# Kernel optimization log

Measured on AMD Instinct MI355X. Metric: run time of the kernel, lower is better.

## Reference

```python
import jax, jax.numpy as jnp
from jax import lax
import numpy as np

S, ST, CI, K = 3, 2, 64, 7  # num_subset_S, num_subset_T, inter_channels, kernel_size


def _ln2(x, g, b, eps=1e-5):
    # LayerNorm over the last TWO dims (matches normalized_shape=[L, C])
    m = x.mean(axis=(-2, -1), keepdims=True)
    v = x.var(axis=(-2, -1), keepdims=True)
    return (x - m) / jnp.sqrt(v + eps) * g + b


def setup_inputs() -> dict:
    key = jax.random.key(0)
    ks = jax.random.split(key, 8)
    N, V, T, C = 32, 25, 64, 256
    g = lambda i, shape: jax.random.normal(ks[i], shape, jnp.float32) * 0.02
    return {
        "x": jax.random.normal(ks[0], (N, V, T, C), jnp.float32),
        "Wqk_s": g(1, (C, 2 * S * CI)), "bqk_s": jnp.zeros((2 * S * CI,), jnp.float32),
        "alphas": jnp.ones((1, 1, 1, S), jnp.float32),
        "attention0s": jnp.ones((1, V, V, S), jnp.float32) / V,
        "Wo_s": g(2, (S * C, C)), "bo_s": jnp.zeros((C,), jnp.float32),
        "g_os": jnp.ones((T, C), jnp.float32), "b_os": jnp.zeros((T, C), jnp.float32),
        "Wff_s": g(3, (C, C)), "bff_s": jnp.zeros((C,), jnp.float32),
        "g_ffs": jnp.ones((T, C), jnp.float32), "b_ffs": jnp.zeros((T, C), jnp.float32),
        "Wqk_t": g(4, (C, 4 * ST * CI)), "bqk_t": jnp.zeros((4 * ST * CI,), jnp.float32),
        "alphat_f": jnp.ones((1, 1, 1, ST), jnp.float32),
        "alphat_b": jnp.ones((1, 1, 1, ST), jnp.float32),
        "Wo_t": g(5, (2 * ST * C, C)), "bo_t": jnp.zeros((C,), jnp.float32),
        "g_ot": jnp.ones((V, C), jnp.float32), "b_ot": jnp.zeros((V, C), jnp.float32),
        "Wff_t": g(6, (C, C)), "bff_t": jnp.zeros((C,), jnp.float32),
        "g_fft": jnp.ones((V, C), jnp.float32), "b_fft": jnp.zeros((V, C), jnp.float32),
        "conv_w": g(7, (C, C, K, 1)), "conv_b": jnp.zeros((C,), jnp.float32),
        "bn_g": jnp.ones((C,), jnp.float32), "bn_b": jnp.zeros((C,), jnp.float32),
        "bn_m": jnp.zeros((C,), jnp.float32), "bn_v": jnp.ones((C,), jnp.float32),
    }


def reference(x, Wqk_s, bqk_s, alphas, attention0s, Wo_s, bo_s, g_os, b_os,
              Wff_s, bff_s, g_ffs, b_ffs, Wqk_t, bqk_t, alphat_f, alphat_b,
              Wo_t, bo_t, g_ot, b_ot, Wff_t, bff_t, g_fft, b_fft,
              conv_w, conv_b, bn_g, bn_b, bn_m, bn_v):
    N, V, T, C = x.shape
    gelu = lambda a: jax.nn.gelu(a, approximate=False)
    # ---- spatial multi-subset attention ----
    qk = (x @ Wqk_s + bqk_s).reshape(N, V, T, CI, 2 * S)
    q, k = qk[..., :S], qk[..., S:]
    att = jnp.tanh(jnp.einsum('nutcs,nvtcs->nuvs', q, k) / (CI * T)) * alphas + attention0s
    y = jnp.einsum('nutc,nuvs->nvtcs', x, att).reshape(N, V, T, S * C)
    y = gelu(x + _ln2(y @ Wo_s + bo_s, g_os, b_os))       # out_nets + residual (downs1=id)
    y = gelu(x + _ln2(y @ Wff_s + bff_s, g_ffs, b_ffs))   # ff_nets  + residual (downs2=id)
    y = y.transpose(0, 2, 1, 3)                            # (N,T,V,C)
    # ---- directed temporal attention ----
    qkt = (y @ Wqk_t + bqk_t).reshape(N, T, V, CI, 4 * ST)
    q_f, q_b = qkt[..., :ST], qkt[..., ST:2 * ST]
    k_f, k_b = qkt[..., 2 * ST:3 * ST], qkt[..., 3 * ST:]
    bmask = jnp.triu(jnp.ones((T, T), x.dtype))            # backward_mask; forward = transpose
    att_b = jnp.tanh(jnp.einsum('ntvcs,nqvcs->ntqs', q_b, k_b) / (CI * V)) * alphat_b * bmask[None, :, :, None]
    att_f = jnp.tanh(jnp.einsum('ntvcs,nqvcs->ntqs', q_f, k_f) / (CI * V)) * alphat_f * bmask.T[None, :, :, None]
    z_f = jnp.einsum('ntvc,ntqs->nqvcs', y, att_f).reshape(N, T, V, ST * C)
    z_b = jnp.einsum('ntvc,ntqs->nqvcs', y, att_b).reshape(N, T, V, ST * C)
    z = jnp.concatenate([z_f, z_b], axis=-1)               # (N,T,V,4C)
    z = gelu(y + _ln2(z @ Wo_t + bo_t, g_ot, b_ot))        # out_nett + residual (downt1=id)
    z = gelu(y + _ln2(z @ Wff_t + bff_t, g_fft, b_fft))    # ff_nett  + residual (downt2=id)
    # ---- TCN tail: (N,T,V,C) -> nctv ----
    zc = z.transpose(0, 3, 1, 2)                           # (N,C,T,V)
    pad = (K - 1) // 2
    z1 = lax.conv_general_dilated(zc, conv_w, (1, 1), [(pad, pad), (0, 0)],
                                  dimension_numbers=('NCHW', 'OIHW', 'NCHW'))
    z1 = z1 + conv_b[None, :, None, None]
    z1 = (z1 - bn_m[None, :, None, None]) / jnp.sqrt(bn_v + 1e-5)[None, :, None, None]
    z1 = z1 * bn_g[None, :, None, None] + bn_b[None, :, None, None]  # BatchNorm2d (eval)
    z1 = gelu(zc + z1)                                     # downt3 = identity
    return z1.transpose(0, 3, 2, 1)                        # nctv -> nvtc, (N,V,T,C)
```

## Files before the change

### kernel.cpp

```cpp
#include <hip/hip_runtime.h>

static constexpr int N_ = 32, V_ = 25, T_ = 64, C_ = 256;
static constexpr int S_ = 3, ST_ = 2, CI_ = 64, K_ = 7;
static constexpr int M_  = N_ * V_ * T_;
static constexpr int TC_ = T_ * C_;
static constexpr int VC_ = V_ * C_;
static constexpr long TOT_ = (long)M_ * C_;
static constexpr long PLANE_ = 2048L * 1600;
static constexpr int TP_ = T_ + 6;

typedef __bf16 bf16x8 __attribute__((ext_vector_type(8)));
typedef float  f32x4  __attribute__((ext_vector_type(4)));

__device__ __forceinline__ float gelu_f(float x) {
    return 0.5f * x * (1.0f + erff(x * 0.70710678118654752f));
}
__device__ __forceinline__ ushort f2bf(float x) {
    uint u = __float_as_uint(x);
    u += 0x7fffu + ((u >> 16) & 1u);
    return (ushort)(u >> 16);
}
__device__ __forceinline__ float bf2f(ushort h) { return __uint_as_float((uint)h << 16); }

__device__ __forceinline__ int lofs(int row, int chunk) {
    return row * 32 + ((chunk ^ ((row >> 1) & 3)) << 3);
}

__device__ __forceinline__ void gll16(const ushort* g, ushort* l) {
    __builtin_amdgcn_global_load_lds(
        (const __attribute__((address_space(1))) void*)g,
        (__attribute__((address_space(3))) void*)l, 16, 0, 0);
}

__device__ __forceinline__ void xcd_swz(int& bx, int& by) {
    const int gx = gridDim.x;
    const int nwg = gx * gridDim.y;
    const int o = blockIdx.y * gx + blockIdx.x;
    const int q = nwg >> 3, r = nwg & 7;
    const int xcd = o & 7, idx = o >> 3;
    const int id = (xcd < r) ? (xcd * (q + 1) + idx)
                             : (r * (q + 1) + (xcd - r) * q + idx);
    bx = id % gx; by = id / gx;
}

__global__ void prep_w(const float* __restrict__ W, int Kc, int Nc,
                       ushort* __restrict__ hi, ushort* __restrict__ lo) {
    int idx = blockIdx.x * 256 + threadIdx.x;
    if (idx >= Kc * Nc) return;
    int n = idx / Kc, k = idx % Kc;
    float x = W[(long)k * Nc + n];
    ushort h = f2bf(x);
    hi[idx] = h;
    lo[idx] = f2bf(x - bf2f(h));
}
__global__ void prep_conv(const float* __restrict__ cw,
                          ushort* __restrict__ hi, ushort* __restrict__ lo) {
    int idx = blockIdx.x * 256 + threadIdx.x;
    if (idx >= K_ * C_ * C_) return;
    int kh = idx / (C_ * C_);
    int rem = idx % (C_ * C_);
    int o = rem >> 8, i = rem & 255;
    float x = cw[((long)o * C_ + i) * K_ + kh];
    ushort h = f2bf(x);
    hi[idx] = h;
    lo[idx] = f2bf(x - bf2f(h));
}
__global__ void prep_x(const float* __restrict__ X,
                       ushort* __restrict__ Xh, ushort* __restrict__ Xl) {
    long i = (long)blockIdx.x * 256 + threadIdx.x;
    if (i >= TOT_) return;
    float v = X[i];
    ushort h = f2bf(v);
    Xh[i] = h;
    Xl[i] = f2bf(v - bf2f(h));
}
__global__ void zero_pad(ushort* __restrict__ Zph, ushort* __restrict__ Zpl) {
    int idx = blockIdx.x * 256 + threadIdx.x;
    if (idx >= N_ * 6 * V_ * C_) return;
    int n = idx / (6 * V_ * C_);
    int rem = idx % (6 * V_ * C_);
    int tpi = rem / (V_ * C_), vc = rem % (V_ * C_);
    int tp = (tpi < 3) ? tpi : (64 + tpi);
    long o = ((long)(n * TP_ + tp) * V_) * C_ + vc;
    Zph[o] = 0; Zpl[o] = 0;
}

__global__ __launch_bounds__(256) void gemm_bf(
    const ushort* __restrict__ Agh, const ushort* __restrict__ Agl,
    const ushort* __restrict__ Wh,  const ushort* __restrict__ Wl,
    const float* __restrict__ bias,
    float* __restrict__ Out, int Nc)
{
    __shared__ ushort Ah[128 * 32], Al[128 * 32], Bh[128 * 32], Bl[128 * 32];
    int bx, by;  xcd_swz(bx, by);
    const int tid = threadIdx.x;
    const int row0 = by * 128, col0 = bx * 128;
    const int lane = tid & 63;
    const int wid = tid >> 6, wm = wid >> 1, wn = wid & 1;
    const int fr = lane & 15, fc = lane >> 4;
    const int r0 = tid >> 2;
    const int cl0 = (tid & 3) ^ ((r0 >> 1) & 3);
    const int r1 = r0 + 64;
    const int cl1 = (tid & 3) ^ ((r1 >> 1) & 3);
    const long a0off = (long)(row0 + r0) * 256 + cl0 * 8;
    const long a1off = (long)(row0 + r1) * 256 + cl1 * 8;
    const long w0off = (long)(col0 + r0) * 256 + cl0 * 8;
    const long w1off = (long)(col0 + r1) * 256 + cl1 * 8;
    ushort* dA0 = &Ah[tid * 8];         ushort* dA1 = &Ah[(tid + 256) * 8];
    ushort* dL0 = &Al[tid * 8];         ushort* dL1 = &Al[(tid + 256) * 8];
    ushort* dB0 = &Bh[tid * 8];         ushort* dB1 = &Bh[(tid + 256) * 8];
    ushort* dM0 = &Bl[tid * 8];         ushort* dM1 = &Bl[(tid + 256) * 8];

    f32x4 acc[4][4] = {};
    for (int k0 = 0; k0 < 256; k0 += 32) {
        __syncthreads();
        gll16(Agh + a0off + k0, dA0);  gll16(Agh + a1off + k0, dA1);
        gll16(Agl + a0off + k0, dL0);  gll16(Agl + a1off + k0, dL1);
        gll16(Wh  + w0off + k0, dB0);  gll16(Wh  + w1off + k0, dB1);
        gll16(Wl  + w0off + k0, dM0);  gll16(Wl  + w1off + k0, dM1);
        __syncthreads();
        bf16x8 fah[4], fal[4];
        #pragma unroll
        for (int i = 0; i < 4; ++i) {
            int oA = lofs(wm * 64 + i * 16 + fr, fc);
            fah[i] = *(bf16x8*)&Ah[oA];
            fal[i] = *(bf16x8*)&Al[oA];
        }
        #pragma unroll
        for (int j = 0; j < 4; ++j) {
            int oW = lofs(wn * 64 + j * 16 + fr, fc);
            bf16x8 wh = *(bf16x8*)&Bh[oW];
            bf16x8 wl = *(bf16x8*)&Bl[oW];
            #pragma unroll
            for (int i = 0; i < 4; ++i) {
                acc[i][j] = __builtin_amdgcn_mfma_f32_16x16x32_bf16(fah[i], wh, acc[i][j], 0, 0, 0);
                acc[i][j] = __builtin_amdgcn_mfma_f32_16x16x32_bf16(fah[i], wl, acc[i][j], 0, 0, 0);
                acc[i][j] = __builtin_amdgcn_mfma_f32_16x16x32_bf16(fal[i], wh, acc[i][j], 0, 0, 0);
            }
        }
    }
    float bv[4]; int colv[4];
    #pragma unroll
    for (int j = 0; j < 4; ++j) {
        colv[j] = col0 + wn * 64 + j * 16 + fr;
        bv[j] = bias ? bias[colv[j]] : 0.0f;
    }
    #pragma unroll
    for (int i = 0; i < 4; ++i) {
        long rbase = row0 + wm * 64 + i * 16 + fc * 4;
        #pragma unroll
        for (int r = 0; r < 4; ++r) {
            long ob = (rbase + r) * (long)Nc;
            #pragma unroll
            for (int j = 0; j < 4; ++j)
                Out[ob + colv[j]] = acc[i][j][r] + bv[j];
        }
    }
}

__global__ __launch_bounds__(256) void conv_bn_gelu(
    const ushort* __restrict__ Zph, const ushort* __restrict__ Zpl,
    const ushort* __restrict__ Wh, const ushort* __restrict__ Wl,
    const float* __restrict__ conv_b, const float* __restrict__ bn_g,
    const float* __restrict__ bn_b,  const float* __restrict__ bn_m,
    const float* __restrict__ bn_v,
    float* __restrict__ Out)
{
    __shared__ ushort Ah[128 * 32], Al[128 * 32], Bh[128 * 32], Bl[128 * 32];
    int bx, by;  xcd_swz(bx, by);
    const int tid = threadIdx.x;
    const int row0 = by * 128, col0 = bx * 128;
    const int lane = tid & 63;
    const int wid = tid >> 6, wm = wid >> 1, wn = wid & 1;
    const int fr = lane & 15, fc = lane >> 4;
    const int r0 = tid >> 2;
    const int cl0 = (tid & 3) ^ ((r0 >> 1) & 3);
    const int r1 = r0 + 64;
    const int cl1 = (tid & 3) ^ ((r1 >> 1) & 3);
    const int m0 = row0 + r0, m1 = row0 + r1;
    const int n0 = m0 / (T_ * V_), q0 = m0 % (T_ * V_);
    const int n1 = m1 / (T_ * V_), q1 = m1 % (T_ * V_);
    const long a0base = ((long)(n0 * TP_ + q0 / V_) * V_ + q0 % V_) * 256 + cl0 * 8;
    const long a1base = ((long)(n1 * TP_ + q1 / V_) * V_ + q1 % V_) * 256 + cl1 * 8;
    const long w0base = (long)(col0 + r0) * 256 + cl0 * 8;
    const long w1base = (long)(col0 + r1) * 256 + cl1 * 8;
    ushort* dA0 = &Ah[tid * 8];         ushort* dA1 = &Ah[(tid + 256) * 8];
    ushort* dL0 = &Al[tid * 8];         ushort* dL1 = &Al[(tid + 256) * 8];
    ushort* dB0 = &Bh[tid * 8];         ushort* dB1 = &Bh[(tid + 256) * 8];
    ushort* dM0 = &Bl[tid * 8];         ushort* dM1 = &Bl[(tid + 256) * 8];

    f32x4 acc[4][4] = {};
    for (int kt = 0; kt < K_ * 8; ++kt) {
        const int kh = kt >> 3;
        const long kc = (kt & 7) * 32;
        const long ao = (long)kh * V_ * 256;
        const long wo = (long)kh * 65536 + kc;
        __syncthreads();
        gll16(Zph + a0base + ao + kc, dA0);  gll16(Zph + a1base + ao + kc, dA1);
        gll16(Zpl + a0base + ao + kc, dL0);  gll16(Zpl + a1base + ao + kc, dL1);
        gll16(Wh + w0base + wo, dB0);        gll16(Wh + w1base + wo, dB1);
        gll16(Wl + w0base + wo, dM0);        gll16(Wl + w1base + wo, dM1);
        __syncthreads();
        bf16x8 fah[4], fal[4];
        #pragma unroll
        for (int i = 0; i < 4; ++i) {
            int oA = lofs(wm * 64 + i * 16 + fr, fc);
            fah[i] = *(bf16x8*)&Ah[oA];
            fal[i] = *(bf16x8*)&Al[oA];
        }
        #pragma unroll
        for (int j = 0; j < 4; ++j) {
            int oW = lofs(wn * 64 + j * 16 + fr, fc);
            bf16x8 wh = *(bf16x8*)&Bh[oW];
            bf16x8 wl = *(bf16x8*)&Bl[oW];
            #pragma unroll
            for (int i = 0; i < 4; ++i) {
                acc[i][j] = __builtin_amdgcn_mfma_f32_16x16x32_bf16(fah[i], wh, acc[i][j], 0, 0, 0);
                acc[i][j] = __builtin_amdgcn_mfma_f32_16x16x32_bf16(fah[i], wl, acc[i][j], 0, 0, 0);
                acc[i][j] = __builtin_amdgcn_mfma_f32_16x16x32_bf16(fal[i], wh, acc[i][j], 0, 0, 0);
            }
        }
    }
    float cbv[4], scv[4], shv[4]; int colv[4];
    #pragma unroll
    for (int j = 0; j < 4; ++j) {
        int c = col0 + wn * 64 + j * 16 + fr;
        colv[j] = c;
        cbv[j] = conv_b[c];
        float sc = rsqrtf(bn_v[c] + 1e-5f) * bn_g[c];
        scv[j] = sc;
        shv[j] = bn_b[c] - bn_m[c] * sc;
    }
    #pragma unroll
    for (int i = 0; i < 4; ++i)
        #pragma unroll
        for (int r = 0; r < 4; ++r) {
            int m = row0 + wm * 64 + i * 16 + fc * 4 + r;
            int n = m / (T_ * V_);
            int rem = m % (T_ * V_);
            int t = rem / V_, v = rem % V_;
            long ob = (((long)n * V_ + v) * T_ + t) * C_;
            long pb = ((long)(n * TP_ + t + 3) * V_ + v) * C_;
            #pragma unroll
            for (int j = 0; j < 4; ++j) {
                float cv = acc[i][j][r] + cbv[j];
                float bn = cv * scv[j] + shv[j];
                float res = bf2f(Zph[pb + colv[j]]) + bf2f(Zpl[pb + colv[j]]);
                Out[ob + colv[j]] = gelu_f(res + bn);
            }
        }
}

__global__ void zero_f32(float* __restrict__ p, int n) {
    int i = blockIdx.x * 256 + threadIdx.x;
    if (i < n) p[i] = 0.0f;
}

__global__ __launch_bounds__(256) void att_s_partial(
    const float* __restrict__ QK,
    float* __restrict__ attPre)
{
    const int n = blockIdx.x;
    const int tg = blockIdx.y;
    __shared__ float lds[V_ * 385];
    const int NOUT = V_ * V_ * S_;
    float acc[8] = {};
    for (int ttc = 0; ttc < 4; ++ttc) {
        int t = tg * 4 + ttc;
        __syncthreads();
        for (int l = threadIdx.x; l < V_ * 96; l += 256) {
            int v = l / 96, j = (l % 96) * 4;
            float4 q = *(const float4*)&QK[(((long)n * V_ + v) * T_ + t) * 384 + j];
            float* d = &lds[v * 385 + j];
            d[0] = q.x; d[1] = q.y; d[2] = q.z; d[3] = q.w;
        }
        __syncthreads();
        int ai = 0;
        for (int o = threadIdx.x; o < NOUT; o += 256, ++ai) {
            int u = o / (V_ * S_), rem = o % (V_ * S_), v = rem / S_, s = rem % S_;
            const float* qp = &lds[u * 385 + s];
            const float* kp = &lds[v * 385 + S_ + s];
            float sum = 0.f;
            #pragma unroll 8
            for (int ci = 0; ci < CI_; ++ci) sum += qp[ci * 6] * kp[ci * 6];
            acc[ai] += sum;
        }
    }
    int ai = 0;
    for (int o = threadIdx.x; o < NOUT; o += 256, ++ai)
        atomicAdd(&attPre[(long)n * NOUT + o], acc[ai]);
}

__global__ void att_s_final(const float* __restrict__ attPre,
                            const float* __restrict__ alphas,
                            const float* __restrict__ att0,
                            float* __restrict__ attS) {
    int idx = blockIdx.x * 256 + threadIdx.x;
    if (idx >= N_ * V_ * V_ * S_) return;
    int o = idx % (V_ * V_ * S_);
    int s = o % S_;
    attS[idx] = tanhf(attPre[idx] * (1.0f / (CI_ * T_))) * alphas[s] + att0[o];
}

__global__ __launch_bounds__(256) void vmix_all(
    const float* __restrict__ G,
    const float* __restrict__ attS,
    const float* __restrict__ bias,
    float* __restrict__ P)
{
    const int n = blockIdx.y;
    const int t = blockIdx.x;
    const int c = threadIdx.x;
    __shared__ float a[3][V_ * V_];
    for (int l = threadIdx.x; l < V_ * V_ * S_; l += 256) {
        int uv = l / S_, s = l % S_;
        a[s][uv] = attS[((long)n * V_ * V_ + uv) * S_ + s];
    }
    __syncthreads();
    float acc[V_] = {};
    for (int u = 0; u < V_; ++u) {
        const float* g = G + ((long)((n * V_ + u) * T_) + t) * 768 + c;
        float v0 = g[0], v1 = g[256], v2 = g[512];
        const float* a0 = &a[0][u * V_], *a1 = &a[1][u * V_], *a2 = &a[2][u * V_];
        #pragma unroll
        for (int v = 0; v < V_; ++v)
            acc[v] += a0[v] * v0 + a1[v] * v1 + a2[v] * v2;
    }
    const float b = bias[c];
    for (int v = 0; v < V_; ++v)
        P[((long)(n * V_ + v) * T_ + t) * C_ + c] = acc[v] + b;
}

__global__ void qkt_repack(const float* __restrict__ QKT,
                           ushort* __restrict__ QPh, ushort* __restrict__ QPl) {
    long idx = (long)blockIdx.x * 256 + threadIdx.x;
    if (idx >= (long)M_ * CI_) return;
    int m = (int)(idx >> 6), ci = (int)(idx & 63);
    int n = m / (T_ * V_);
    int rem = m % (T_ * V_);
    int t = rem / V_, v = rem % V_;
    const float* src = QKT + (long)m * 512 + ci * 8;
    float4 s0 = *(const float4*)src;
    float4 s1 = *(const float4*)(src + 4);
    float f[8] = {s0.x, s0.y, s0.z, s0.w, s1.x, s1.y, s1.z, s1.w};
    long rowk = ((long)(n * T_ + t)) * 1600 + v * 64 + ci;
    #pragma unroll
    for (int chan = 0; chan < 8; ++chan) {
        ushort h = f2bf(f[chan]);
        QPh[(long)chan * PLANE_ + rowk] = h;
        QPl[(long)chan * PLANE_ + rowk] = f2bf(f[chan] - bf2f(h));
    }
}

__global__ __launch_bounds__(256) void att_t_mfma(
    const ushort* __restrict__ QPh, const ushort* __restrict__ QPl,
    float* __restrict__ part)
{
    const int ks = blockIdx.x, pair = blockIdx.y, n = blockIdx.z;
    const int kbeg = (ks * 50) / 4, kend = ((ks + 1) * 50) / 4;
    __shared__ ushort Qh[64 * 32], Ql[64 * 32], Kh[64 * 32], Kl[64 * 32];
    const int tid = threadIdx.x;
    const int lane = tid & 63;
    const int wid = tid >> 6, wm = wid >> 1, wn = wid & 1;
    const int fr = lane & 15, fc = lane >> 4;
    const int tr = tid >> 2, tc = tid & 3;
    const long rowoff = ((long)n * T_ + tr) * 1600 + tc * 8;
    const ushort* qh_g = QPh + (long)pair * PLANE_ + rowoff;
    const ushort* ql_g = QPl + (long)pair * PLANE_ + rowoff;
    const ushort* kh_g = QPh + (long)(pair + 4) * PLANE_ + rowoff;
    const ushort* kl_g = QPl + (long)(pair + 4) * PLANE_ + rowoff;
    const int la = lofs(tr, tc);

    uint4 pqh = *(const uint4*)(qh_g + kbeg * 32);
    uint4 pql = *(const uint4*)(ql_g + kbeg * 32);
    uint4 pkh = *(const uint4*)(kh_g + kbeg * 32);
    uint4 pkl = *(const uint4*)(kl_g + kbeg * 32);

    f32x4 acc[2][2] = {};
    for (int kstep = kbeg; kstep < kend; ++kstep) {
        __syncthreads();
        *(uint4*)&Qh[la] = pqh;  *(uint4*)&Ql[la] = pql;
        *(uint4*)&Kh[la] = pkh;  *(uint4*)&Kl[la] = pkl;
        __syncthreads();
        if (kstep + 1 < kend) {
            pqh = *(const uint4*)(qh_g + (kstep + 1) * 32);
            pql = *(const uint4*)(ql_g + (kstep + 1) * 32);
            pkh = *(const uint4*)(kh_g + (kstep + 1) * 32);
            pkl = *(const uint4*)(kl_g + (kstep + 1) * 32);
        }
        bf16x8 ah[2], al[2];
        #pragma unroll
        for (int i = 0; i < 2; ++i) {
            int oA = lofs(wm * 32 + i * 16 + fr, fc);
            ah[i] = *(bf16x8*)&Qh[oA];
            al[i] = *(bf16x8*)&Ql[oA];
        }
        #pragma unroll
        for (int j = 0; j < 2; ++j) {
            int oB = lofs(wn * 32 + j * 16 + fr, fc);
            bf16x8 bh = *(bf16x8*)&Kh[oB];
            bf16x8 bl = *(bf16x8*)&Kl[oB];
            #pragma unroll
            for (int i = 0; i < 2; ++i) {
                acc[i][j] = __builtin_amdgcn_mfma_f32_16x16x32_bf16(ah[i], bh, acc[i][j], 0, 0, 0);
                acc[i][j] = __builtin_amdgcn_mfma_f32_16x16x32_bf16(ah[i], bl, acc[i][j], 0, 0, 0);
                acc[i][j] = __builtin_amdgcn_mfma_f32_16x16x32_bf16(al[i], bh, acc[i][j], 0, 0, 0);
            }
        }
    }
    float* pb = part + (((long)ks * N_ + n) * 4 + pair) * 4096;
    #pragma unroll
    for (int i = 0; i < 2; ++i)
        #pragma unroll
        for (int r = 0; r < 4; ++r) {
            int t = wm * 32 + i * 16 + fc * 4 + r;
            #pragma unroll
            for (int j = 0; j < 2; ++j) {
                int q = wn * 32 + j * 16 + fr;
                pb[t * 64 + q] = acc[i][j][r];
            }
        }
}

__global__ void att_t_final(const float* __restrict__ part,
                            const float* __restrict__ alphat_f,
                            const float* __restrict__ alphat_b,
                            float* __restrict__ attF, float* __restrict__ attB) {
    int idx = blockIdx.x * 256 + threadIdx.x;
    if (idx >= N_ * 4 * 4096) return;
    int n = idx >> 14;
    int rem = idx & 16383;
    int p = rem >> 12, tq = rem & 4095;
    int t = tq >> 6, q = tq & 63;
    const long stride = (long)N_ * 4 * 4096;
    float sum = 0.f;
    #pragma unroll
    for (int ks = 0; ks < 4; ++ks) sum += part[ks * stride + idx];
    float val = tanhf(sum * (1.0f / (CI_ * V_)));
    if (p < 2) {
        float m = (t >= q) ? 1.0f : 0.0f;
        attF[((long)(n * 2 + p)) * 4096 + tq] = val * alphat_f[p] * m;
    } else {
        float m = (q >= t) ? 1.0f : 0.0f;
        attB[((long)(n * 2 + (p - 2))) * 4096 + tq] = val * alphat_b[p - 2] * m;
    }
}

template <bool INIT>
__global__ __launch_bounds__(256) void tmix_all(
    const float* __restrict__ G,
    const float* __restrict__ att,
    const float* __restrict__ bias,
    float* __restrict__ P)
{
    const int n = blockIdx.y;
    const int col = blockIdx.x * 64 + (threadIdx.x & 63);
    const int ty = threadIdx.x >> 6;
    const int v = col >> 8, c = col & 255;
    __shared__ float a[2 * T_ * T_];
    for (int l = threadIdx.x; l < 2 * T_ * T_; l += 256)
        a[l] = att[(long)n * 2 * T_ * T_ + l];
    __syncthreads();
    float acc[16] = {};
    for (int t = 0; t < T_; ++t) {
        const float* g = G + ((long)((n * T_ + t) * V_) + v) * 512 + c;
        float v0 = g[0], v1 = g[256];
        const float* ar0 = &a[t * T_ + ty * 16];
        const float* ar1 = ar0 + T_ * T_;
        #pragma unroll
        for (int i = 0; i < 16; ++i) acc[i] += ar0[i] * v0 + ar1[i] * v1;
    }
    for (int i = 0; i < 16; ++i) {
        int q = ty * 16 + i;
        long idx = ((long)n * T_ + q) * VC_ + col;
        if (INIT) P[idx] = acc[i] + bias[c];
        else      P[idx] += acc[i];
    }
}

#define LN_STATS(PBASE, L)                                                     \
    float s = 0.f, ss = 0.f;                                                   \
    for (int i = threadIdx.x; i < L; i += 256) { float a = (PBASE)[i]; s += a; ss += a * a; } \
    __shared__ float rs[4], rss[4];                                            \
    _Pragma("unroll")                                                          \
    for (int off = 32; off > 0; off >>= 1) { s += __shfl_down(s, off); ss += __shfl_down(ss, off); } \
    if ((threadIdx.x & 63) == 0) { rs[threadIdx.x >> 6] = s; rss[threadIdx.x >> 6] = ss; } \
    __syncthreads();                                                           \
    s = rs[0] + rs[1] + rs[2] + rs[3];                                         \
    ss = rss[0] + rss[1] + rss[2] + rss[3];                                    \
    const float mean = s * (1.0f / (L));                                       \
    const float var  = ss * (1.0f / (L)) - mean * mean;                        \
    const float rstd = rsqrtf(var + 1e-5f);

__global__ __launch_bounds__(256) void ln_tc_y(
    const float* __restrict__ P, const float* __restrict__ X,
    const float* __restrict__ G, const float* __restrict__ B,
    ushort* __restrict__ Oh, ushort* __restrict__ Ol)
{
    const int g = blockIdx.x;
    const float* p = P + (long)g * TC_;
    const float* x = X + (long)g * TC_;
    LN_STATS(p, TC_)
    for (int i = threadIdx.x; i < TC_; i += 256) {
        float val = (p[i] - mean) * rstd * G[i] + B[i];
        float r = gelu_f(x[i] + val);
        ushort h = f2bf(r);
        Oh[(long)g * TC_ + i] = h;
        Ol[(long)g * TC_ + i] = f2bf(r - bf2f(h));
    }
}

__global__ __launch_bounds__(256) void ln_tc_yt(
    const float* __restrict__ P, const float* __restrict__ X,
    const float* __restrict__ G, const float* __restrict__ B,
    ushort* __restrict__ Oh, ushort* __restrict__ Ol)
{
    const int g = blockIdx.x;
    const int n = g / V_, v = g % V_;
    const float* p = P + (long)g * TC_;
    const float* x = X + (long)g * TC_;
    LN_STATS(p, TC_)
    for (int i = threadIdx.x; i < TC_; i += 256) {
        float val = (p[i] - mean) * rstd * G[i] + B[i];
        float r = gelu_f(x[i] + val);
        int t = i >> 8, c = i & 255;
        long o = (((long)n * T_ + t) * V_ + v) * C_ + c;
        ushort h = f2bf(r);
        Oh[o] = h;
        Ol[o] = f2bf(r - bf2f(h));
    }
}

__global__ __launch_bounds__(256) void ln_vc_z(
    const float* __restrict__ P,
    const ushort* __restrict__ Xh, const ushort* __restrict__ Xl,
    const float* __restrict__ G, const float* __restrict__ B,
    ushort* __restrict__ Oh, ushort* __restrict__ Ol)
{
    const int g = blockIdx.x;
    const float* p = P + (long)g * VC_;
    LN_STATS(p, VC_)
    for (int i = threadIdx.x; i < VC_; i += 256) {
        long o = (long)g * VC_ + i;
        float xr = bf2f(Xh[o]) + bf2f(Xl[o]);
        float val = (p[i] - mean) * rstd * G[i] + B[i];
        float r = gelu_f(xr + val);
        ushort h = f2bf(r);
        Oh[o] = h;
        Ol[o] = f2bf(r - bf2f(h));
    }
}

__global__ __launch_bounds__(256) void ln_vc_z2(
    const float* __restrict__ P,
    const ushort* __restrict__ Xh, const ushort* __restrict__ Xl,
    const float* __restrict__ G, const float* __restrict__ B,
    ushort* __restrict__ Zph, ushort* __restrict__ Zpl)
{
    const int g = blockIdx.x;
    const int n = g / T_, t = g % T_;
    const float* p = P + (long)g * VC_;
    LN_STATS(p, VC_)
    const long pbase = ((long)(n * TP_ + t + 3) * V_) * C_;
    for (int i = threadIdx.x; i < VC_; i += 256) {
        long o = (long)g * VC_ + i;
        float xr = bf2f(Xh[o]) + bf2f(Xl[o]);
        float val = (p[i] - mean) * rstd * G[i] + B[i];
        float r = gelu_f(xr + val);
        ushort h = f2bf(r);
        Zph[pbase + i] = h;
        Zpl[pbase + i] = f2bf(r - bf2f(h));
    }
}

extern "C" void kernel_launch(void* const* d_in, const int* in_sizes, int n_in,
                              void* d_out, int out_size, void* d_ws, size_t ws_size,
                              hipStream_t stream)
{
    const float* x        = (const float*)d_in[0];
    const float* Wqk_s    = (const float*)d_in[1];
    const float* bqk_s    = (const float*)d_in[2];
    const float* alphas   = (const float*)d_in[3];
    const float* att0s    = (const float*)d_in[4];
    const float* Wo_s     = (const float*)d_in[5];
    const float* bo_s     = (const float*)d_in[6];
    const float* g_os     = (const float*)d_in[7];
    const float* b_os     = (const float*)d_in[8];
    const float* Wff_s    = (const float*)d_in[9];
    const float* bff_s    = (const float*)d_in[10];
    const float* g_ffs    = (const float*)d_in[11];
    const float* b_ffs    = (const float*)d_in[12];
    const float* Wqk_t    = (const float*)d_in[13];
    const float* bqk_t    = (const float*)d_in[14];
    const float* alphat_f = (const float*)d_in[15];
    const float* alphat_b = (const float*)d_in[16];
    const float* Wo_t     = (const float*)d_in[17];
    const float* bo_t     = (const float*)d_in[18];
    const float* g_ot     = (const float*)d_in[19];
    const float* b_ot     = (const float*)d_in[20];
    const float* Wff_t    = (const float*)d_in[21];
    const float* bff_t    = (const float*)d_in[22];
    const float* g_fft    = (const float*)d_in[23];
    const float* b_fft    = (const float*)d_in[24];
    const float* conv_w   = (const float*)d_in[25];
    const float* conv_b   = (const float*)d_in[26];
    const float* bn_g     = (const float*)d_in[27];
    const float* bn_b     = (const float*)d_in[28];
    const float* bn_m     = (const float*)d_in[29];
    const float* bn_v     = (const float*)d_in[30];

    float* Bp  = (float*)d_ws;
    float* R0f = Bp;
    float* R1f = Bp + TOT_;
    float* R2f = Bp + 2 * TOT_;
    float* R3f = Bp + 3 * TOT_;
    float* SM  = Bp + 4 * TOT_;
    float* attPre = SM;
    float* attS   = attPre + N_*V_*V_*S_;
    float* attF   = attS   + N_*V_*V_*S_;
    float* attB   = attF   + (long)N_*2*T_*T_;
    float* part   = attB   + (long)N_*2*T_*T_;
    ushort* wp = (ushort*)(part + 4L*N_*4*4096);
    ushort* qs_h = wp;  wp += 384*256;   ushort* qs_l = wp;  wp += 384*256;
    ushort* os_h = wp;  wp += 768*256;   ushort* os_l = wp;  wp += 768*256;
    ushort* fs_h = wp;  wp += 256*256;   ushort* fs_l = wp;  wp += 256*256;
    ushort* qt_h = wp;  wp += 512*256;   ushort* qt_l = wp;  wp += 512*256;
    ushort* ot0_h= wp;  wp += 512*256;   ushort* ot0_l= wp;  wp += 512*256;
    ushort* ot1_h= wp;  wp += 512*256;   ushort* ot1_l= wp;  wp += 512*256;
    ushort* ft_h = wp;  wp += 256*256;   ushort* ft_l = wp;  wp += 256*256;
    ushort* cv_h = wp;  wp += K_*256*256; ushort* cv_l = wp;

    ushort* xh  = (ushort*)R3f;  ushort* xl  = xh  + TOT_;
    ushort* Yh  = (ushort*)R0f;  ushort* Yl  = Yh  + TOT_;
    ushort* YTh = (ushort*)d_out; ushort* YTl = YTh + TOT_;
    ushort* QPh = (ushort*)R2f;  ushort* QPl = (ushort*)R3f;
    ushort* Zh  = (ushort*)R0f;  ushort* Zl  = Zh  + TOT_;
    ushort* Zph = (ushort*)R1f;
    ushort* Zpl = Zph + (long)N_ * TP_ * V_ * C_;

    auto prepw = [&](const float* W, int Nc, ushort* h, ushort* l) {
        prep_w<<<(256*Nc + 255)/256, 256, 0, stream>>>(W, 256, Nc, h, l);
    };
    prepw(Wqk_s, 384, qs_h, qs_l);
    prepw(Wo_s,  768, os_h, os_l);
    prepw(Wff_s, 256, fs_h, fs_l);
    prepw(Wqk_t, 512, qt_h, qt_l);
    prepw(Wo_t,                   512, ot0_h, ot0_l);
    prepw(Wo_t + (long)ST_*C_*C_, 512, ot1_h, ot1_l);
    prepw(Wff_t, 256, ft_h, ft_l);
    prep_conv<<<(K_*C_*C_ + 255)/256, 256, 0, stream>>>(conv_w, cv_h, cv_l);
    prep_x<<<(int)((TOT_ + 255)/256), 256, 0, stream>>>(x, xh, xl);

    gemm_bf<<<dim3(3, 400), 256, 0, stream>>>(xh, xl, qs_h, qs_l, bqk_s, R0f, 384);
    zero_f32<<<(N_*V_*V_*S_ + 255)/256, 256, 0, stream>>>(attPre, N_*V_*V_*S_);
    att_s_partial<<<dim3(N_, 16), 256, 0, stream>>>(R0f, attPre);
    att_s_final<<<(N_*V_*V_*S_ + 255)/256, 256, 0, stream>>>(attPre, alphas, att0s, attS);
    gemm_bf<<<dim3(6, 400), 256, 0, stream>>>(xh, xl, os_h, os_l, nullptr, R0f, 768);
    vmix_all<<<dim3(T_, N_), 256, 0, stream>>>(R0f, attS, bo_s, R3f);
    ln_tc_y<<<N_*V_, 256, 0, stream>>>(R3f, x, g_os, b_os, Yh, Yl);
    gemm_bf<<<dim3(2, 400), 256, 0, stream>>>(Yh, Yl, fs_h, fs_l, bff_s, R1f, 256);
    ln_tc_yt<<<N_*V_, 256, 0, stream>>>(R1f, x, g_ffs, b_ffs, YTh, YTl);

    gemm_bf<<<dim3(4, 400), 256, 0, stream>>>(YTh, YTl, qt_h, qt_l, bqk_t, R0f, 512);
    qkt_repack<<<(int)(((long)M_*CI_ + 255)/256), 256, 0, stream>>>(R0f, QPh, QPl);
    att_t_mfma<<<dim3(4, 4, N_), 256, 0, stream>>>(QPh, QPl, part);
    att_t_final<<<(N_*4*4096 + 255)/256, 256, 0, stream>>>(part, alphat_f, alphat_b, attF, attB);
    gemm_bf<<<dim3(4, 400), 256, 0, stream>>>(YTh, YTl, ot0_h, ot0_l, nullptr, R0f, 512);
    tmix_all<true><<<dim3(VC_/64, N_), 256, 0, stream>>>(R0f, attF, bo_t, R2f);
    gemm_bf<<<dim3(4, 400), 256, 0, stream>>>(YTh, YTl, ot1_h, ot1_l, nullptr, R0f, 512);
    tmix_all<false><<<dim3(VC_/64, N_), 256, 0, stream>>>(R0f, attB, nullptr, R2f);
    ln_vc_z<<<N_*T_, 256, 0, stream>>>(R2f, YTh, YTl, g_ot, b_ot, Zh, Zl);
    gemm_bf<<<dim3(2, 400), 256, 0, stream>>>(Zh, Zl, ft_h, ft_l, bff_t, R3f, 256);
    zero_pad<<<(N_*6*V_*C_ + 255)/256, 256, 0, stream>>>(Zph, Zpl);
    ln_vc_z2<<<N_*T_, 256, 0, stream>>>(R3f, YTh, YTl, g_fft, b_fft, Zph, Zpl);

    conv_bn_gelu<<<dim3(2, 400), 256, 0, stream>>>(Zph, Zpl, cv_h, cv_l, conv_b, bn_g, bn_b, bn_m, bn_v, (float*)d_out);
}
```

Measured before the change: 1.266 ms.

## Double-buffer LDS in GEMM and conv kernels, merge weight-prep launches

The bf16 split-precision GEMM and the conv GEMM now use two LDS buffers per operand, so the global-to-LDS load of the next K slice is issued before the MFMAs on the current slice. This drops one of the two barriers per iteration and aims to hide load latency behind compute. The eight weight-preparation launches are merged into one kernel that dispatches on a flat index, which removes launch overhead. LDS use doubles to 64 KB per block, which may lower occupancy.

```diff
diff --git a/kernel.cpp b/kernel.cpp
--- a/kernel.cpp
+++ b/kernel.cpp
@@ -43,27 +43,45 @@
     bx = id % gx; by = id / gx;
 }
 
-__global__ void prep_w(const float* __restrict__ W, int Kc, int Nc,
-                       ushort* __restrict__ hi, ushort* __restrict__ lo) {
+__global__ void prep_weights(
+    const float* __restrict__ Wqk_s, const float* __restrict__ Wo_s,
+    const float* __restrict__ Wff_s, const float* __restrict__ Wqk_t,
+    const float* __restrict__ Wo_t,  const float* __restrict__ Wff_t,
+    const float* __restrict__ conv_w,
+    ushort* __restrict__ qs_h, ushort* __restrict__ qs_l,
+    ushort* __restrict__ os_h, ushort* __restrict__ os_l,
+    ushort* __restrict__ fs_h, ushort* __restrict__ fs_l,
+    ushort* __restrict__ qt_h, ushort* __restrict__ qt_l,
+    ushort* __restrict__ ot0_h, ushort* __restrict__ ot0_l,
+    ushort* __restrict__ ot1_h, ushort* __restrict__ ot1_l,
+    ushort* __restrict__ ft_h, ushort* __restrict__ ft_l,
+    ushort* __restrict__ cv_h, ushort* __restrict__ cv_l)
+{
     int idx = blockIdx.x * 256 + threadIdx.x;
-    if (idx >= Kc * Nc) return;
-    int n = idx / Kc, k = idx % Kc;
-    float x = W[(long)k * Nc + n];
-    ushort h = f2bf(x);
-    hi[idx] = h;
-    lo[idx] = f2bf(x - bf2f(h));
-}
-__global__ void prep_conv(const float* __restrict__ cw,
-                          ushort* __restrict__ hi, ushort* __restrict__ lo) {
-    int idx = blockIdx.x * 256 + threadIdx.x;
-    if (idx >= K_ * C_ * C_) return;
-    int kh = idx / (C_ * C_);
-    int rem = idx % (C_ * C_);
-    int o = rem >> 8, i = rem & 255;
-    float x = cw[((long)o * C_ + i) * K_ + kh];
-    ushort h = f2bf(x);
-    hi[idx] = h;
-    lo[idx] = f2bf(x - bf2f(h));
+    float x; ushort *h, *l; int li;
+    if (idx < 819200) {
+        const float* W; int base, ldw;
+        if      (idx <  98304) { W=Wqk_s; h=qs_h;  l=qs_l;  base=0;      ldw=384; }
+        else if (idx < 294912) { W=Wo_s;  h=os_h;  l=os_l;  base=98304;  ldw=768; }
+        else if (idx < 360448) { W=Wff_s; h=fs_h;  l=fs_l;  base=294912; ldw=256; }
+        else if (idx < 491520) { W=Wqk_t; h=qt_h;  l=qt_l;  base=360448; ldw=512; }
+        else if (idx < 622592) { W=Wo_t;  h=ot0_h; l=ot0_l; base=491520; ldw=512; }
+        else if (idx < 753664) { W=Wo_t + (long)ST_*C_*C_; h=ot1_h; l=ot1_l; base=622592; ldw=512; }
+        else                   { W=Wff_t; h=ft_h;  l=ft_l;  base=753664; ldw=256; }
+        li = idx - base;
+        int n = li >> 8, k = li & 255;
+        x = W[(long)k * ldw + n];
+    } else {
+        li = idx - 819200;
+        int kh = li / (C_ * C_);
+        int rem = li % (C_ * C_);
+        int o = rem >> 8, i = rem & 255;
+        x = conv_w[((long)o * C_ + i) * K_ + kh];
+        h = cv_h; l = cv_l;
+    }
+    ushort hb = f2bf(x);
+    h[li] = hb;
+    l[li] = f2bf(x - bf2f(hb));
 }
 __global__ void prep_x(const float* __restrict__ X,
                        ushort* __restrict__ Xh, ushort* __restrict__ Xl) {
@@ -91,7 +109,8 @@
     const float* __restrict__ bias,
     float* __restrict__ Out, int Nc)
 {
-    __shared__ ushort Ah[128 * 32], Al[128 * 32], Bh[128 * 32], Bl[128 * 32];
+    __shared__ ushort Ah[2][128 * 32], Al[2][128 * 32];
+    __shared__ ushort Bh[2][128 * 32], Bl[2][128 * 32];
     int bx, by;  xcd_swz(bx, by);
     const int tid = threadIdx.x;
     const int row0 = by * 128, col0 = bx * 128;
@@ -106,31 +125,33 @@
     const long a1off = (long)(row0 + r1) * 256 + cl1 * 8;
     const long w0off = (long)(col0 + r0) * 256 + cl0 * 8;
     const long w1off = (long)(col0 + r1) * 256 + cl1 * 8;
-    ushort* dA0 = &Ah[tid * 8];         ushort* dA1 = &Ah[(tid + 256) * 8];
-    ushort* dL0 = &Al[tid * 8];         ushort* dL1 = &Al[(tid + 256) * 8];
-    ushort* dB0 = &Bh[tid * 8];         ushort* dB1 = &Bh[(tid + 256) * 8];
-    ushort* dM0 = &Bl[tid * 8];         ushort* dM1 = &Bl[(tid + 256) * 8];
+    const int u0 = tid * 8, u1 = (tid + 256) * 8;
+
+    auto stage = [&](int b, int k0) {
+        gll16(Agh + a0off + k0, &Ah[b][u0]);  gll16(Agh + a1off + k0, &Ah[b][u1]);
+        gll16(Agl + a0off + k0, &Al[b][u0]);  gll16(Agl + a1off + k0, &Al[b][u1]);
+        gll16(Wh  + w0off + k0, &Bh[b][u0]);  gll16(Wh  + w1off + k0, &Bh[b][u1]);
+        gll16(Wl  + w0off + k0, &Bl[b][u0]);  gll16(Wl  + w1off + k0, &Bl[b][u1]);
+    };
 
     f32x4 acc[4][4] = {};
-    for (int k0 = 0; k0 < 256; k0 += 32) {
-        __syncthreads();
-        gll16(Agh + a0off + k0, dA0);  gll16(Agh + a1off + k0, dA1);
-        gll16(Agl + a0off + k0, dL0);  gll16(Agl + a1off + k0, dL1);
-        gll16(Wh  + w0off + k0, dB0);  gll16(Wh  + w1off + k0, dB1);
-        gll16(Wl  + w0off + k0, dM0);  gll16(Wl  + w1off + k0, dM1);
-        __syncthreads();
+    stage(0, 0);
+    __syncthreads();
+    int cur = 0;
+    for (int ks = 0; ks < 8; ++ks) {
+        if (ks + 1 < 8) stage(cur ^ 1, (ks + 1) * 32);
         bf16x8 fah[4], fal[4];
         #pragma unroll
         for (int i = 0; i < 4; ++i) {
             int oA = lofs(wm * 64 + i * 16 + fr, fc);
-            fah[i] = *(bf16x8*)&Ah[oA];
-            fal[i] = *(bf16x8*)&Al[oA];
+            fah[i] = *(bf16x8*)&Ah[cur][oA];
+            fal[i] = *(bf16x8*)&Al[cur][oA];
         }
         #pragma unroll
         for (int j = 0; j < 4; ++j) {
             int oW = lofs(wn * 64 + j * 16 + fr, fc);
-            bf16x8 wh = *(bf16x8*)&Bh[oW];
-            bf16x8 wl = *(bf16x8*)&Bl[oW];
+            bf16x8 wh = *(bf16x8*)&Bh[cur][oW];
+            bf16x8 wl = *(bf16x8*)&Bl[cur][oW];
             #pragma unroll
             for (int i = 0; i < 4; ++i) {
                 acc[i][j] = __builtin_amdgcn_mfma_f32_16x16x32_bf16(fah[i], wh, acc[i][j], 0, 0, 0);
@@ -138,6 +159,8 @@
                 acc[i][j] = __builtin_amdgcn_mfma_f32_16x16x32_bf16(fal[i], wh, acc[i][j], 0, 0, 0);
             }
         }
+        __syncthreads();
+        cur ^= 1;
     }
     float bv[4]; int colv[4];
     #pragma unroll
@@ -166,7 +189,8 @@
     const float* __restrict__ bn_v,
     float* __restrict__ Out)
 {
-    __shared__ ushort Ah[128 * 32], Al[128 * 32], Bh[128 * 32], Bl[128 * 32];
+    __shared__ ushort Ah[2][128 * 32], Al[2][128 * 32];
+    __shared__ ushort Bh[2][128 * 32], Bl[2][128 * 32];
     int bx, by;  xcd_swz(bx, by);
     const int tid = threadIdx.x;
     const int row0 = by * 128, col0 = bx * 128;
@@ -184,35 +208,41 @@
     const long a1base = ((long)(n1 * TP_ + q1 / V_) * V_ + q1 % V_) * 256 + cl1 * 8;
     const long w0base = (long)(col0 + r0) * 256 + cl0 * 8;
     const long w1base = (long)(col0 + r1) * 256 + cl1 * 8;
-    ushort* dA0 = &Ah[tid * 8];         ushort* dA1 = &Ah[(tid + 256) * 8];
-    ushort* dL0 = &Al[tid * 8];         ushort* dL1 = &Al[(tid + 256) * 8];
-    ushort* dB0 = &Bh[tid * 8];         ushort* dB1 = &Bh[(tid + 256) * 8];
-    ushort* dM0 = &Bl[tid * 8];         ushort* dM1 = &Bl[(tid + 256) * 8];
-
-    f32x4 acc[4][4] = {};
-    for (int kt = 0; kt < K_ * 8; ++kt) {
+    const int u0 = tid * 8, u1 = (tid + 256) * 8;
+
+    auto stage = [&](int b, int kt) {
         const int kh = kt >> 3;
         const long kc = (kt & 7) * 32;
         const long ao = (long)kh * V_ * 256;
         const long wo = (long)kh * 65536 + kc;
-        __syncthreads();
-        gll16(Zph + a0base + ao + kc, dA0);  gll16(Zph + a1base + ao + kc, dA1);
-        gll16(Zpl + a0base + ao + kc, dL0);  gll16(Zpl + a1base + ao + kc, dL1);
-        gll16(Wh + w0base + wo, dB0);        gll16(Wh + w1base + wo, dB1);
-        gll16(Wl + w0base + wo, dM0);        gll16(Wl + w1base + wo, dM1);
-        __syncthreads();
+        gll16(Zph + a0base + ao + kc, &Ah[b][u0]);
+        gll16(Zph + a1base + ao + kc, &Ah[b][u1]);
+        gll16(Zpl + a0base + ao + kc, &Al[b][u0]);
+        gll16(Zpl + a1base + ao + kc, &Al[b][u1]);
+        gll16(Wh + w0base + wo, &Bh[b][u0]);
+        gll16(Wh + w1base + wo, &Bh[b][u1]);
+        gll16(Wl + w0base + wo, &Bl[b][u0]);
+        gll16(Wl + w1base + wo, &Bl[b][u1]);
+    };
+
+    f32x4 acc[4][4] = {};
+    stage(0, 0);
+    __syncthreads();
+    int cur = 0;
+    for (int kt = 0; kt < K_ * 8; ++kt) {
+        if (kt + 1 < K_ * 8) stage(cur ^ 1, kt + 1);
         bf16x8 fah[4], fal[4];
         #pragma unroll
         for (int i = 0; i < 4; ++i) {
             int oA = lofs(wm * 64 + i * 16 + fr, fc);
-            fah[i] = *(bf16x8*)&Ah[oA];
-            fal[i] = *(bf16x8*)&Al[oA];
+            fah[i] = *(bf16x8*)&Ah[cur][oA];
+            fal[i] = *(bf16x8*)&Al[cur][oA];
         }
         #pragma unroll
         for (int j = 0; j < 4; ++j) {
             int oW = lofs(wn * 64 + j * 16 + fr, fc);
-            bf16x8 wh = *(bf16x8*)&Bh[oW];
-            bf16x8 wl = *(bf16x8*)&Bl[oW];
+            bf16x8 wh = *(bf16x8*)&Bh[cur][oW];
+            bf16x8 wl = *(bf16x8*)&Bl[cur][oW];
             #pragma unroll
             for (int i = 0; i < 4; ++i) {
                 acc[i][j] = __builtin_amdgcn_mfma_f32_16x16x32_bf16(fah[i], wh, acc[i][j], 0, 0, 0);
@@ -220,6 +250,8 @@
                 acc[i][j] = __builtin_amdgcn_mfma_f32_16x16x32_bf16(fal[i], wh, acc[i][j], 0, 0, 0);
             }
         }
+        __syncthreads();
+        cur ^= 1;
     }
     float cbv[4], scv[4], shv[4]; int colv[4];
     #pragma unroll
@@ -638,17 +670,10 @@
     ushort* Zph = (ushort*)R1f;
     ushort* Zpl = Zph + (long)N_ * TP_ * V_ * C_;
 
-    auto prepw = [&](const float* W, int Nc, ushort* h, ushort* l) {
-        prep_w<<<(256*Nc + 255)/256, 256, 0, stream>>>(W, 256, Nc, h, l);
-    };
-    prepw(Wqk_s, 384, qs_h, qs_l);
-    prepw(Wo_s,  768, os_h, os_l);
-    prepw(Wff_s, 256, fs_h, fs_l);
-    prepw(Wqk_t, 512, qt_h, qt_l);
-    prepw(Wo_t,                   512, ot0_h, ot0_l);
-    prepw(Wo_t + (long)ST_*C_*C_, 512, ot1_h, ot1_l);
-    prepw(Wff_t, 256, ft_h, ft_l);
-    prep_conv<<<(K_*C_*C_ + 255)/256, 256, 0, stream>>>(conv_w, cv_h, cv_l);
+    prep_weights<<<4992, 256, 0, stream>>>(
+        Wqk_s, Wo_s, Wff_s, Wqk_t, Wo_t, Wff_t, conv_w,
+        qs_h, qs_l, os_h, os_l, fs_h, fs_l, qt_h, qt_l,
+        ot0_h, ot0_l, ot1_h, ot1_l, ft_h, ft_l, cv_h, cv_l);
     prep_x<<<(int)((TOT_ + 255)/256), 256, 0, stream>>>(x, xh, xl);
 
     gemm_bf<<<dim3(3, 400), 256, 0, stream>>>(xh, xl, qs_h, qs_l, bqk_s, R0f, 384);
```

Result: no change. 1.260 ms (-0.5%).
